# Optimization experiments

Hardware: AMD Instinct MI355X
Metric: run time of the kernel (lower is better)

## Reference

```python
import jax, jax.numpy as jnp
import numpy as np

BATCH = 16384
MODEL_DIM = 768
SAE_HIDDEN = 16384
K = 3


def setup_inputs() -> dict:
    key = jax.random.key(0)
    k1, k2, k3, k4, k5 = jax.random.split(key, 5)
    scale_enc = 1.0 / np.sqrt(MODEL_DIM)
    scale_dec = 1.0 / np.sqrt(SAE_HIDDEN)
    return {
        "model_activations": jax.random.normal(k1, (BATCH, MODEL_DIM), jnp.float32),
        "W_enc": jax.random.normal(k2, (SAE_HIDDEN, MODEL_DIM), jnp.float32) * scale_enc,
        "b_enc": jax.random.normal(k3, (SAE_HIDDEN,), jnp.float32) * scale_enc,
        "W_dec": jax.random.normal(k4, (MODEL_DIM, SAE_HIDDEN), jnp.float32) * scale_dec,
        "b_dec": jax.random.normal(k5, (MODEL_DIM,), jnp.float32) * scale_dec,
    }


def reference(model_activations, W_enc, b_enc, W_dec, b_dec):
    # encoder linear: [B, D] @ [D, H] + [H] -> [B, H]
    pre_activations = model_activations @ W_enc.T + b_enc
    # top-k (k=3) per row
    topk_vals, topk_idx = jax.lax.top_k(pre_activations, K)  # [B, K]
    # scatter the k values into a zero tensor (sparse activation)
    B = pre_activations.shape[0]
    rows = jnp.arange(B)[:, None]  # [B, 1]
    sae_activations = jnp.zeros_like(pre_activations).at[rows, topk_idx].set(topk_vals)
    # number of unique live latents across the whole batch (static-shape version of torch.unique)
    live_mask = jnp.zeros((pre_activations.shape[1],), dtype=jnp.bool_).at[topk_idx.reshape(-1)].set(True)
    num_live_latents = jnp.sum(live_mask.astype(jnp.int32))
    # decoder linear: [B, H] @ [H, D] + [D] -> [B, D]
    reconstructed = sae_activations @ W_dec.T + b_dec
    return reconstructed, num_live_latents
```

## Files before the change

### kernel.cpp

```cpp
#include <hip/hip_runtime.h>
#include <cstdint>
#include <cstddef>

#define B_ROWS 16384
#define DIM    768
#define HID    16384
#define NCB    128
#define KSTEPS (DIM / 32)

typedef __bf16 bf16x8 __attribute__((ext_vector_type(8)));
typedef float  f32x4  __attribute__((ext_vector_type(4)));
typedef unsigned int   u32;
typedef unsigned short u16;

__device__ __forceinline__ u32 umaxu(u32 a, u32 b) { return a > b ? a : b; }
__device__ __forceinline__ u32 uminu(u32 a, u32 b) { return a < b ? a : b; }

__device__ __forceinline__ int swz(int r) { return (r & 3) ^ ((r >> 2) & 3); }

__device__ __forceinline__ u16 f2bf(float f) {
    u32 u = __float_as_uint(f);
    return (u16)((u + 0x7FFFu + ((u >> 16) & 1u)) >> 16);
}

__device__ __forceinline__ u32 pk(float v, int gidx) {
    u32 b = __float_as_uint(v);
    u32 t = b >> 16;
    t ^= (b & 0x80000000u) ? 0xFFFFu : 0x8000u;
    return (t << 16) | (u32)gidx;
}

__device__ __forceinline__ void gll16(const void* g, void* l) {
    __builtin_amdgcn_global_load_lds(
        (const __attribute__((address_space(1))) unsigned int*)g,
        (__attribute__((address_space(3))) unsigned int*)l, 16, 0, 0);
}

__device__ __forceinline__ bool better(float v1, int i1, float v2, int i2) {
    return (v1 > v2) || (v1 == v2 && i1 < i2);
}
__device__ __forceinline__ void ins3(float v, int i,
                                     float& v0, int& i0, float& v1, int& i1,
                                     float& v2, int& i2) {
    if (better(v, i, v2, i2)) {
        v2 = v; i2 = i;
        if (better(v2, i2, v1, i1)) { float tv = v1; int ti = i1; v1 = v2; i1 = i2; v2 = tv; i2 = ti; }
        if (better(v1, i1, v0, i0)) { float tv = v0; int ti = i0; v0 = v1; i0 = i1; v1 = tv; i1 = ti; }
    }
}

__global__ __launch_bounds__(256) void cast_bf16(const float* __restrict__ X,
                                                 const float* __restrict__ W,
                                                 u16* __restrict__ Xb, u16* __restrict__ Wb) {
    const int n4 = (B_ROWS * DIM) / 4;
    for (int i = blockIdx.x * blockDim.x + threadIdx.x; i < n4; i += gridDim.x * blockDim.x) {
        float4 x = ((const float4*)X)[i];
        float4 w = ((const float4*)W)[i];
        ushort4 xo, wo;
        xo.x = f2bf(x.x); xo.y = f2bf(x.y); xo.z = f2bf(x.z); xo.w = f2bf(x.w);
        wo.x = f2bf(w.x); wo.y = f2bf(w.y); wo.z = f2bf(w.z); wo.w = f2bf(w.w);
        ((ushort4*)Xb)[i] = xo;
        ((ushort4*)Wb)[i] = wo;
    }
}

__global__ __launch_bounds__(256) void gemm_screen(const u16* __restrict__ Xb,
                                                   const u16* __restrict__ Wb,
                                                   const float* __restrict__ benc,
                                                   u32* __restrict__ pvpi) {
    __shared__ __align__(16) u16 As[128 * 32];
    __shared__ __align__(16) u16 Bs[128 * 32];
    __shared__ u32 sm[4 * 64 * 3];

    const int bid = blockIdx.x;
    const int st = bid >> 8, loc = bid & 255;
    const int rb = (st >> 3) * 16 + (loc >> 4);
    const int cb = (st & 7) * 16 + (loc & 15);
    const int rowBase = rb * 128, colBase = cb * 128;

    const int tid = threadIdx.x;
    const int w = tid >> 6, lane = tid & 63;

    const u16* gA[2]; const u16* gB[2]; u16* lA[2]; u16* lB[2];
#pragma unroll
    for (int i = 0; i < 2; i++) {
        const int q = w * 2 + i;
        const int p = q * 64 + lane;
        const int r = p >> 2;
        const int c = (p & 3) ^ swz(r);
        gA[i] = Xb + (size_t)(rowBase + r) * DIM + c * 8;
        gB[i] = Wb + (size_t)(colBase + r) * DIM + c * 8;
        lA[i] = As + q * 512;
        lB[i] = Bs + q * 512;
    }

    const int j = lane & 15, g = lane >> 4;
    const int wm = (w >> 1) * 64, wn = (w & 1) * 64;
    int aoff[4], boff[4];
#pragma unroll
    for (int t = 0; t < 4; t++) {
        const int m = wm + t * 16 + j;
        aoff[t] = m * 4 + (g ^ swz(m));
        const int n = wn + t * 16 + j;
        boff[t] = n * 4 + (g ^ swz(n));
    }

    f32x4 acc[4][4];
#pragma unroll
    for (int mt = 0; mt < 4; mt++)
#pragma unroll
        for (int nt = 0; nt < 4; nt++) acc[mt][nt] = (f32x4){0.f, 0.f, 0.f, 0.f};

#pragma unroll
    for (int i = 0; i < 2; i++) { gll16(gA[i], lA[i]); gll16(gB[i], lB[i]); }

    const bf16x8* As8 = (const bf16x8*)As;
    const bf16x8* Bs8 = (const bf16x8*)Bs;

    for (int kk = 0; kk < KSTEPS; ++kk) {
        __syncthreads();
        bf16x8 aF[4], bF[4];
#pragma unroll
        for (int t = 0; t < 4; t++) { aF[t] = As8[aoff[t]]; bF[t] = Bs8[boff[t]]; }
        __syncthreads();
        if (kk + 1 < KSTEPS) {
            const int o = (kk + 1) * 32;
#pragma unroll
            for (int i = 0; i < 2; i++) { gll16(gA[i] + o, lA[i]); gll16(gB[i] + o, lB[i]); }
        }
#pragma unroll
        for (int mt = 0; mt < 4; mt++)
#pragma unroll
            for (int nt = 0; nt < 4; nt++)
                acc[mt][nt] = __builtin_amdgcn_mfma_f32_16x16x32_bf16(aF[mt], bF[nt], acc[mt][nt], 0, 0, 0);
    }

    float bias[4]; int gcol[4];
#pragma unroll
    for (int nt = 0; nt < 4; nt++) {
        gcol[nt] = colBase + wn + nt * 16 + j;
        bias[nt] = benc[gcol[nt]];
    }

#pragma unroll
    for (int mt = 0; mt < 4; mt++) {
#pragma unroll
        for (int reg = 0; reg < 4; reg++) {
            const u32 k0 = pk(acc[mt][0][reg] + bias[0], gcol[0]);
            const u32 k1 = pk(acc[mt][1][reg] + bias[1], gcol[1]);
            const u32 k2 = pk(acc[mt][2][reg] + bias[2], gcol[2]);
            const u32 k3 = pk(acc[mt][3][reg] + bias[3], gcol[3]);
            u32 a0 = umaxu(k0, k1), a1 = uminu(k0, k1);
            u32 b0 = umaxu(k2, k3), b1 = uminu(k2, k3);
            u32 x0 = umaxu(a0, b0);
            u32 p = uminu(a0, b0), q = umaxu(a1, b1), r2 = uminu(a1, b1);
            u32 x1 = umaxu(p, q);
            u32 x2 = umaxu(uminu(p, q), r2);
#pragma unroll
            for (int mk = 1; mk < 16; mk <<= 1) {
                const u32 y0 = (u32)__shfl_xor((int)x0, mk, 64);
                const u32 y1 = (u32)__shfl_xor((int)x1, mk, 64);
                const u32 y2 = (u32)__shfl_xor((int)x2, mk, 64);
                const u32 P = uminu(x0, y0), Q = umaxu(x1, y1);
                const u32 R = uminu(x1, y1), S = umaxu(x2, y2);
                const u32 z0 = umaxu(x0, y0);
                const u32 z1 = umaxu(P, Q);
                const u32 z2 = umaxu(umaxu(uminu(P, Q), R), S);
                x0 = z0; x1 = z1; x2 = z2;
            }
            if ((lane & 15) == 0) {
                const int rloc = mt * 16 + g * 4 + reg;
                sm[(w * 64 + rloc) * 3 + 0] = x0;
                sm[(w * 64 + rloc) * 3 + 1] = x1;
                sm[(w * 64 + rloc) * 3 + 2] = x2;
            }
        }
    }
    __syncthreads();
    if (tid < 128) {
        const int row = tid;
        const int wp = (row >> 6) * 2, rl = row & 63;
        const u32 A0 = sm[((wp + 0) * 64 + rl) * 3 + 0];
        const u32 A1 = sm[((wp + 0) * 64 + rl) * 3 + 1];
        const u32 A2 = sm[((wp + 0) * 64 + rl) * 3 + 2];
        const u32 B0 = sm[((wp + 1) * 64 + rl) * 3 + 0];
        const u32 B1 = sm[((wp + 1) * 64 + rl) * 3 + 1];
        const u32 B2 = sm[((wp + 1) * 64 + rl) * 3 + 2];
        const u32 P = uminu(A0, B0), Q = umaxu(A1, B1);
        const u32 R = uminu(A1, B1), S = umaxu(A2, B2);
        const u32 z0 = umaxu(A0, B0);
        const u32 z1 = umaxu(P, Q);
        const u32 z2 = umaxu(umaxu(uminu(P, Q), R), S);
        const size_t base = ((size_t)(rowBase + row) * NCB + cb) * 3;
        pvpi[base + 0] = z0; pvpi[base + 1] = z1; pvpi[base + 2] = z2;
    }
}

__global__ __launch_bounds__(256) void reduce_recheck(
        const u32* __restrict__ pvpi, const float* __restrict__ X,
        const float* __restrict__ Wenc, const float* __restrict__ benc,
        float* __restrict__ fv, int* __restrict__ fi, int* __restrict__ mask) {
    const int wid = threadIdx.x >> 6, lane = threadIdx.x & 63;
    const int row = blockIdx.x * 4 + wid;

    const u32* p = pvpi + (size_t)row * (NCB * 3);
    u32 k[6];
#pragma unroll
    for (int t = 0; t < 6; t++) k[t] = p[t * 64 + lane];

    u32 cand[16];
#pragma unroll
    for (int it = 0; it < 16; ++it) {
        u32 m = k[0];
#pragma unroll
        for (int t = 1; t < 6; t++) m = umaxu(m, k[t]);
#pragma unroll
        for (int mk = 1; mk < 64; mk <<= 1) m = umaxu(m, (u32)__shfl_xor((int)m, mk, 64));
        cand[it] = m;
#pragma unroll
        for (int t = 0; t < 6; t++) if (k[t] == m) k[t] = 0;
    }

    const float4* xp = (const float4*)(X + (size_t)row * DIM) + lane * 3;
    const float4 x0 = xp[0], x1 = xp[1], x2 = xp[2];

    float v0 = -INFINITY, v1 = -INFINITY, v2 = -INFINITY;
    int   i0 = 0x7fffffff, i1 = 0x7fffffff, i2 = 0x7fffffff;
#pragma unroll
    for (int it = 0; it < 16; ++it) {
        const int ci = (int)(cand[it] & 0xFFFFu);
        const float4* wq = (const float4*)(Wenc + (size_t)ci * DIM) + lane * 3;
        const float4 w0 = wq[0], w1 = wq[1], w2 = wq[2];
        float s = x0.x * w0.x;
        s = fmaf(x0.y, w0.y, s); s = fmaf(x0.z, w0.z, s); s = fmaf(x0.w, w0.w, s);
        s = fmaf(x1.x, w1.x, s); s = fmaf(x1.y, w1.y, s); s = fmaf(x1.z, w1.z, s);
        s = fmaf(x1.w, w1.w, s); s = fmaf(x2.x, w2.x, s); s = fmaf(x2.y, w2.y, s);
        s = fmaf(x2.z, w2.z, s); s = fmaf(x2.w, w2.w, s);
#pragma unroll
        for (int mk = 1; mk < 64; mk <<= 1) s += __shfl_xor(s, mk, 64);
        const float val = s + benc[ci];
        ins3(val, ci, v0, i0, v1, i1, v2, i2);
    }
    if (lane == 0) {
        fv[row * 3 + 0] = v0; fv[row * 3 + 1] = v1; fv[row * 3 + 2] = v2;
        fi[row * 3 + 0] = i0; fi[row * 3 + 1] = i1; fi[row * 3 + 2] = i2;
        mask[i0] = 1; mask[i1] = 1; mask[i2] = 1;
    }
}

__global__ __launch_bounds__(256) void count_live(const int* __restrict__ mask,
                                                  float* __restrict__ outScalar) {
    __shared__ int sd[256];
    const int tid = threadIdx.x;
    int s = 0;
    for (int i = tid; i < HID; i += 256) s += mask[i];
    sd[tid] = s;
    __syncthreads();
    for (int st = 128; st > 0; st >>= 1) {
        if (tid < st) sd[tid] += sd[tid + st];
        __syncthreads();
    }
    if (tid == 0) outScalar[0] = (float)sd[0];
}

__global__ __launch_bounds__(256) void transpose_wdec(const float* __restrict__ W,
                                                      float* __restrict__ Wt) {
    __shared__ float t[32][33];
    const int bx = blockIdx.x;
    const int by = blockIdx.y;
    const int x = threadIdx.x & 31;
    const int y = threadIdx.x >> 5;
#pragma unroll
    for (int i = 0; i < 4; i++) {
        const int d = by * 32 + y + i * 8;
        t[y + i * 8][x] = W[(size_t)d * HID + bx * 32 + x];
    }
    __syncthreads();
#pragma unroll
    for (int i = 0; i < 4; i++) {
        const int h = bx * 32 + y + i * 8;
        Wt[(size_t)h * DIM + by * 32 + x] = t[x][y + i * 8];
    }
}

__global__ __launch_bounds__(192) void decode_rows(
        const float* __restrict__ fv, const int* __restrict__ fi,
        const float* __restrict__ Wt, const float* __restrict__ bdec,
        float* __restrict__ out) {
    const int row = blockIdx.x;
    const int tid = threadIdx.x;
    const float v0 = fv[row * 3 + 0], v1 = fv[row * 3 + 1], v2 = fv[row * 3 + 2];
    const int   i0 = fi[row * 3 + 0], i1 = fi[row * 3 + 1], i2 = fi[row * 3 + 2];
    const int jj = tid * 4;
    const float4 b  = *(const float4*)(bdec + jj);
    const float4 w0 = *(const float4*)(Wt + (size_t)i0 * DIM + jj);
    const float4 w1 = *(const float4*)(Wt + (size_t)i1 * DIM + jj);
    const float4 w2 = *(const float4*)(Wt + (size_t)i2 * DIM + jj);
    float4 o;
    o.x = b.x + v0 * w0.x + v1 * w1.x + v2 * w2.x;
    o.y = b.y + v0 * w0.y + v1 * w1.y + v2 * w2.y;
    o.z = b.z + v0 * w0.z + v1 * w1.z + v2 * w2.z;
    o.w = b.w + v0 * w0.w + v1 * w1.w + v2 * w2.w;
    *(float4*)(out + (size_t)row * DIM + jj) = o;
}

extern "C" void kernel_launch(void* const* d_in, const int* in_sizes, int n_in,
                              void* d_out, int out_size, void* d_ws, size_t ws_size,
                              hipStream_t stream) {
    const float* X    = (const float*)d_in[0];
    const float* Wenc = (const float*)d_in[1];
    const float* benc = (const float*)d_in[2];
    const float* Wdec = (const float*)d_in[3];
    const float* bdec = (const float*)d_in[4];
    float* out = (float*)d_out;

    char* ws = (char*)d_ws;
    u16*   Xb   = (u16*)ws;
    u16*   Wb   = (u16*)(ws + 25165824);
    float* Wt   = (float*)ws;
    u32*   pvpi = (u32*)(ws + 50331648);
    float* fv   = (float*)(ws + 75497472);
    int*   fi   = (int*)(ws + 75694080);
    int*   mask = (int*)(ws + 75890688);

    hipMemsetAsync(mask, 0, HID * sizeof(int), stream);

    cast_bf16<<<3072, 256, 0, stream>>>(X, Wenc, Xb, Wb);
    gemm_screen<<<16384, 256, 0, stream>>>(Xb, Wb, benc, pvpi);
    reduce_recheck<<<B_ROWS / 4, 256, 0, stream>>>(pvpi, X, Wenc, benc, fv, fi, mask);
    count_live<<<1, 256, 0, stream>>>(mask, out + (size_t)B_ROWS * DIM);
    transpose_wdec<<<dim3(HID / 32, DIM / 32), 256, 0, stream>>>(Wdec, Wt);
    decode_rows<<<B_ROWS, 192, 0, stream>>>(fv, fi, Wt, bdec, out);
}
```

Before: 925.8 us.

## Enlarge encoder GEMM tiles to 256x256 with double-buffered pipelined LDS staging

The screening GEMM moves from 128x128x32 tiles with 256 threads to 256x256x64 tiles with 512 threads. LDS is double-buffered with a split-phase schedule that interleaves global-to-LDS loads, LDS reads and MFMA quarters, and MFMA sections run at raised wave priority. Blocks are remapped across 8 groups for cache locality. Halving the column-block count shrinks the candidate buffer and the per-row reduction work in reduce_recheck. The cost is much higher register and LDS pressure and intricate vmcnt/barrier ordering that could limit occupancy or be fragile.

```diff
diff --git a/kernel.cpp b/kernel.cpp
--- a/kernel.cpp
+++ b/kernel.cpp
@@ -5,8 +5,10 @@
 #define B_ROWS 16384
 #define DIM    768
 #define HID    16384
-#define NCB    128
-#define KSTEPS (DIM / 32)
+#define BM     256
+#define BK     64
+#define KT_N   (DIM / BK)
+#define NCB    (HID / BM)
 
 typedef __bf16 bf16x8 __attribute__((ext_vector_type(8)));
 typedef float  f32x4  __attribute__((ext_vector_type(4)));
@@ -15,8 +17,6 @@
 
 __device__ __forceinline__ u32 umaxu(u32 a, u32 b) { return a > b ? a : b; }
 __device__ __forceinline__ u32 uminu(u32 a, u32 b) { return a < b ? a : b; }
-
-__device__ __forceinline__ int swz(int r) { return (r & 3) ^ ((r >> 2) & 3); }
 
 __device__ __forceinline__ u16 f2bf(float f) {
     u32 u = __float_as_uint(f);
@@ -34,6 +34,16 @@
     __builtin_amdgcn_global_load_lds(
         (const __attribute__((address_space(1))) unsigned int*)g,
         (__attribute__((address_space(3))) unsigned int*)l, 16, 0, 0);
+}
+
+__device__ __forceinline__ void merge3(u32& z0, u32& z1, u32& z2,
+                                       u32 A0, u32 A1, u32 A2,
+                                       u32 B0, u32 B1, u32 B2) {
+    const u32 P = uminu(A0, B0), Q = umaxu(A1, B1);
+    const u32 R = uminu(A1, B1), S = umaxu(A2, B2);
+    z0 = umaxu(A0, B0);
+    z1 = umaxu(P, Q);
+    z2 = umaxu(umaxu(uminu(P, Q), R), S);
 }
 
 __device__ __forceinline__ bool better(float v1, int i1, float v2, int i2) {
@@ -64,88 +74,129 @@
     }
 }
 
-__global__ __launch_bounds__(256) void gemm_screen(const u16* __restrict__ Xb,
-                                                   const u16* __restrict__ Wb,
-                                                   const float* __restrict__ benc,
-                                                   u32* __restrict__ pvpi) {
-    __shared__ __align__(16) u16 As[128 * 32];
-    __shared__ __align__(16) u16 Bs[128 * 32];
-    __shared__ u32 sm[4 * 64 * 3];
+__global__ __launch_bounds__(512, 2) void gemm_screen(const u16* __restrict__ Xb,
+                                                      const u16* __restrict__ Wb,
+                                                      const float* __restrict__ benc,
+                                                      u32* __restrict__ pvpi) {
+    __shared__ __align__(16) u16 As[2 * BM * BK];
+    __shared__ __align__(16) u16 Bs[2 * BM * BK];
 
     const int bid = blockIdx.x;
-    const int st = bid >> 8, loc = bid & 255;
-    const int rb = (st >> 3) * 16 + (loc >> 4);
-    const int cb = (st & 7) * 16 + (loc & 15);
-    const int rowBase = rb * 128, colBase = cb * 128;
+    const int wg = ((bid & 7) << 9) | (bid >> 3);
+    const int st = wg >> 8, loc = wg & 255;
+    const int rb = ((st >> 2) << 4) | (loc >> 4);
+    const int cb = ((st & 3) << 4) | (loc & 15);
+    const int rowBase = rb * BM, colBase = cb * BM;
 
     const int tid = threadIdx.x;
-    const int w = tid >> 6, lane = tid & 63;
-
-    const u16* gA[2]; const u16* gB[2]; u16* lA[2]; u16* lB[2];
-#pragma unroll
-    for (int i = 0; i < 2; i++) {
-        const int q = w * 2 + i;
-        const int p = q * 64 + lane;
-        const int r = p >> 2;
-        const int c = (p & 3) ^ swz(r);
-        gA[i] = Xb + (size_t)(rowBase + r) * DIM + c * 8;
-        gB[i] = Wb + (size_t)(colBase + r) * DIM + c * 8;
-        lA[i] = As + q * 512;
-        lB[i] = Bs + q * 512;
-    }
-
+    const int wid = tid >> 6, lane = tid & 63;
+    const int wm = wid >> 2, wn = wid & 3;
     const int j = lane & 15, g = lane >> 4;
-    const int wm = (w >> 1) * 64, wn = (w & 1) * 64;
-    int aoff[4], boff[4];
-#pragma unroll
-    for (int t = 0; t < 4; t++) {
-        const int m = wm + t * 16 + j;
-        aoff[t] = m * 4 + (g ^ swz(m));
-        const int n = wn + t * 16 + j;
-        boff[t] = n * 4 + (g ^ swz(n));
-    }
-
-    f32x4 acc[4][4];
-#pragma unroll
-    for (int mt = 0; mt < 4; mt++)
-#pragma unroll
-        for (int nt = 0; nt < 4; nt++) acc[mt][nt] = (f32x4){0.f, 0.f, 0.f, 0.f};
-
-#pragma unroll
-    for (int i = 0; i < 2; i++) { gll16(gA[i], lA[i]); gll16(gB[i], lB[i]); }
+    const int js = j & 7;
+
+    const int sr = tid >> 3, ss = tid & 7;
+    const int sc = ss ^ (sr & 7);
+    const u32 aoff = (u32)(rowBase + sr) * DIM + (u32)sc * 8;
+    const u32 boff = (u32)(colBase + sr) * DIM + (u32)sc * 8;
+    const int lbw = wid * 512;
+
+#define STAGE_A(H, KTL, D1) do { \
+    gll16(Xb + aoff + (H) * 98304u + (u32)(KTL) * 64u,           As + (D1) * 16384 + (H) * 8192 + lbw); \
+    gll16(Xb + aoff + (H) * 98304u + 49152u + (u32)(KTL) * 64u,  As + (D1) * 16384 + (H) * 8192 + 4096 + lbw); \
+} while (0)
+#define STAGE_B(H, KTL, D1) do { \
+    gll16(Wb + boff + (H) * 98304u + (u32)(KTL) * 64u,           Bs + (D1) * 16384 + (H) * 8192 + lbw); \
+    gll16(Wb + boff + (H) * 98304u + 49152u + (u32)(KTL) * 64u,  Bs + (D1) * 16384 + (H) * 8192 + 4096 + lbw); \
+} while (0)
 
     const bf16x8* As8 = (const bf16x8*)As;
     const bf16x8* Bs8 = (const bf16x8*)Bs;
 
-    for (int kk = 0; kk < KSTEPS; ++kk) {
-        __syncthreads();
-        bf16x8 aF[4], bF[4];
-#pragma unroll
-        for (int t = 0; t < 4; t++) { aF[t] = As8[aoff[t]]; bF[t] = Bs8[boff[t]]; }
-        __syncthreads();
-        if (kk + 1 < KSTEPS) {
-            const int o = (kk + 1) * 32;
-#pragma unroll
-            for (int i = 0; i < 2; i++) { gll16(gA[i] + o, lA[i]); gll16(gB[i] + o, lB[i]); }
-        }
-#pragma unroll
-        for (int mt = 0; mt < 4; mt++)
-#pragma unroll
-            for (int nt = 0; nt < 4; nt++)
-                acc[mt][nt] = __builtin_amdgcn_mfma_f32_16x16x32_bf16(aF[mt], bF[nt], acc[mt][nt], 0, 0, 0);
-    }
+#define READ_A(MH, D) do { \
+    _Pragma("unroll") for (int mtl = 0; mtl < 4; ++mtl) { \
+        const int m8_ = (D) * 2048 + (wm * 128 + ((MH) * 4 + mtl) * 16 + j) * 8; \
+        aF[mtl][0] = As8[m8_ + ((0 + g) ^ js)]; \
+        aF[mtl][1] = As8[m8_ + ((4 + g) ^ js)]; \
+    } } while (0)
+#define READ_B(DST, NH, D) do { \
+    _Pragma("unroll") for (int ntl = 0; ntl < 2; ++ntl) { \
+        const int n8_ = (D) * 2048 + (wn * 64 + ((NH) * 2 + ntl) * 16 + j) * 8; \
+        DST[ntl][0] = Bs8[n8_ + ((0 + g) ^ js)]; \
+        DST[ntl][1] = Bs8[n8_ + ((4 + g) ^ js)]; \
+    } } while (0)
+
+#define MFMA_Q(MH, NH, BF) do { \
+    __builtin_amdgcn_s_setprio(1); \
+    _Pragma("unroll") for (int kk2 = 0; kk2 < 2; ++kk2) \
+    _Pragma("unroll") for (int mtl = 0; mtl < 4; ++mtl) \
+    _Pragma("unroll") for (int ntl = 0; ntl < 2; ++ntl) \
+        acc[(MH) * 4 + mtl][(NH) * 2 + ntl] = __builtin_amdgcn_mfma_f32_16x16x32_bf16( \
+            aF[mtl][kk2], BF[ntl][kk2], acc[(MH) * 4 + mtl][(NH) * 2 + ntl], 0, 0, 0); \
+    __builtin_amdgcn_s_setprio(0); \
+} while (0)
+
+    f32x4 acc[8][4];
+#pragma unroll
+    for (int mt = 0; mt < 8; ++mt)
+#pragma unroll
+        for (int nt = 0; nt < 4; ++nt) acc[mt][nt] = (f32x4){0.f, 0.f, 0.f, 0.f};
+
+    STAGE_A(0, 0, 0); STAGE_B(0, 0, 0); STAGE_B(1, 0, 0); STAGE_A(1, 0, 0);
+    asm volatile("s_waitcnt vmcnt(4)" ::: "memory");
+    __builtin_amdgcn_s_barrier();
+
+    bf16x8 aF[4][2], bLo[2][2], bHi[2][2];
+
+#pragma unroll 1
+    for (int t = 0; t < KT_N; ++t) {
+        const int d = t & 1, d1 = d ^ 1;
+        const bool stg = (t + 1 < KT_N);
+        const int kt = t + 1;
+
+        READ_A(0, d);
+        READ_B(bLo, 0, d);
+        if (stg) STAGE_A(0, kt, d1);
+        __builtin_amdgcn_s_barrier();
+        MFMA_Q(0, 0, bLo);
+        if (stg) asm volatile("s_waitcnt vmcnt(4)" ::: "memory");
+        else     asm volatile("s_waitcnt vmcnt(2)" ::: "memory");
+        __builtin_amdgcn_s_barrier();
+
+        READ_B(bHi, 1, d);
+        if (stg) STAGE_B(0, kt, d1);
+        __builtin_amdgcn_s_barrier();
+        MFMA_Q(0, 1, bHi);
+        if (stg) asm volatile("s_waitcnt vmcnt(4)" ::: "memory");
+        else     asm volatile("s_waitcnt vmcnt(0)" ::: "memory");
+        __builtin_amdgcn_s_barrier();
+
+        READ_A(1, d);
+        if (stg) STAGE_B(1, kt, d1);
+        __builtin_amdgcn_s_barrier();
+        MFMA_Q(1, 1, bHi);
+        __builtin_amdgcn_s_barrier();
+
+        if (stg) STAGE_A(1, kt, d1);
+        __builtin_amdgcn_s_barrier();
+        MFMA_Q(1, 0, bLo);
+        if (stg) asm volatile("s_waitcnt vmcnt(4)" ::: "memory");
+        __builtin_amdgcn_s_barrier();
+    }
+
+    __syncthreads();
+    u32* sm = (u32*)As;
 
     float bias[4]; int gcol[4];
 #pragma unroll
-    for (int nt = 0; nt < 4; nt++) {
-        gcol[nt] = colBase + wn + nt * 16 + j;
+    for (int nt = 0; nt < 4; ++nt) {
+        gcol[nt] = colBase + wn * 64 + nt * 16 + j;
         bias[nt] = benc[gcol[nt]];
     }
 
 #pragma unroll
-    for (int mt = 0; mt < 4; mt++) {
-#pragma unroll
-        for (int reg = 0; reg < 4; reg++) {
+    for (int mt = 0; mt < 8; ++mt) {
+#pragma unroll
+        for (int reg = 0; reg < 4; ++reg) {
             const u32 k0 = pk(acc[mt][0][reg] + bias[0], gcol[0]);
             const u32 k1 = pk(acc[mt][1][reg] + bias[1], gcol[1]);
             const u32 k2 = pk(acc[mt][2][reg] + bias[2], gcol[2]);
@@ -161,39 +212,34 @@
                 const u32 y0 = (u32)__shfl_xor((int)x0, mk, 64);
                 const u32 y1 = (u32)__shfl_xor((int)x1, mk, 64);
                 const u32 y2 = (u32)__shfl_xor((int)x2, mk, 64);
-                const u32 P = uminu(x0, y0), Q = umaxu(x1, y1);
-                const u32 R = uminu(x1, y1), S = umaxu(x2, y2);
-                const u32 z0 = umaxu(x0, y0);
-                const u32 z1 = umaxu(P, Q);
-                const u32 z2 = umaxu(umaxu(uminu(P, Q), R), S);
+                u32 z0, z1, z2;
+                merge3(z0, z1, z2, x0, x1, x2, y0, y1, y2);
                 x0 = z0; x1 = z1; x2 = z2;
             }
             if ((lane & 15) == 0) {
-                const int rloc = mt * 16 + g * 4 + reg;
-                sm[(w * 64 + rloc) * 3 + 0] = x0;
-                sm[(w * 64 + rloc) * 3 + 1] = x1;
-                sm[(w * 64 + rloc) * 3 + 2] = x2;
+                const int row = wm * 128 + mt * 16 + g * 4 + reg;
+                sm[row * 12 + wn * 3 + 0] = x0;
+                sm[row * 12 + wn * 3 + 1] = x1;
+                sm[row * 12 + wn * 3 + 2] = x2;
             }
         }
     }
     __syncthreads();
-    if (tid < 128) {
+    if (tid < 256) {
         const int row = tid;
-        const int wp = (row >> 6) * 2, rl = row & 63;
-        const u32 A0 = sm[((wp + 0) * 64 + rl) * 3 + 0];
-        const u32 A1 = sm[((wp + 0) * 64 + rl) * 3 + 1];
-        const u32 A2 = sm[((wp + 0) * 64 + rl) * 3 + 2];
-        const u32 B0 = sm[((wp + 1) * 64 + rl) * 3 + 0];
-        const u32 B1 = sm[((wp + 1) * 64 + rl) * 3 + 1];
-        const u32 B2 = sm[((wp + 1) * 64 + rl) * 3 + 2];
-        const u32 P = uminu(A0, B0), Q = umaxu(A1, B1);
-        const u32 R = uminu(A1, B1), S = umaxu(A2, B2);
-        const u32 z0 = umaxu(A0, B0);
-        const u32 z1 = umaxu(P, Q);
-        const u32 z2 = umaxu(umaxu(uminu(P, Q), R), S);
+        const u32* s = sm + row * 12;
+        u32 m0, m1, m2, n0, n1, n2, z0, z1, z2;
+        merge3(m0, m1, m2, s[0], s[1], s[2], s[3], s[4], s[5]);
+        merge3(n0, n1, n2, s[6], s[7], s[8], s[9], s[10], s[11]);
+        merge3(z0, z1, z2, m0, m1, m2, n0, n1, n2);
         const size_t base = ((size_t)(rowBase + row) * NCB + cb) * 3;
         pvpi[base + 0] = z0; pvpi[base + 1] = z1; pvpi[base + 2] = z2;
     }
+#undef STAGE_A
+#undef STAGE_B
+#undef READ_A
+#undef READ_B
+#undef MFMA_Q
 }
 
 __global__ __launch_bounds__(256) void reduce_recheck(
@@ -204,21 +250,19 @@
     const int row = blockIdx.x * 4 + wid;
 
     const u32* p = pvpi + (size_t)row * (NCB * 3);
-    u32 k[6];
-#pragma unroll
-    for (int t = 0; t < 6; t++) k[t] = p[t * 64 + lane];
+    u32 k[3];
+#pragma unroll
+    for (int t = 0; t < 3; t++) k[t] = p[t * 64 + lane];
 
     u32 cand[16];
 #pragma unroll
     for (int it = 0; it < 16; ++it) {
-        u32 m = k[0];
-#pragma unroll
-        for (int t = 1; t < 6; t++) m = umaxu(m, k[t]);
+        u32 m = umaxu(umaxu(k[0], k[1]), k[2]);
 #pragma unroll
         for (int mk = 1; mk < 64; mk <<= 1) m = umaxu(m, (u32)__shfl_xor((int)m, mk, 64));
         cand[it] = m;
 #pragma unroll
-        for (int t = 0; t < 6; t++) if (k[t] == m) k[t] = 0;
+        for (int t = 0; t < 3; t++) if (k[t] == m) k[t] = 0;
     }
 
     const float4* xp = (const float4*)(X + (size_t)row * DIM) + lane * 3;
@@ -319,14 +363,14 @@
     u16*   Wb   = (u16*)(ws + 25165824);
     float* Wt   = (float*)ws;
     u32*   pvpi = (u32*)(ws + 50331648);
-    float* fv   = (float*)(ws + 75497472);
-    int*   fi   = (int*)(ws + 75694080);
-    int*   mask = (int*)(ws + 75890688);
+    float* fv   = (float*)(ws + 62914560);
+    int*   fi   = (int*)(ws + 63111168);
+    int*   mask = (int*)(ws + 63307776);
 
     hipMemsetAsync(mask, 0, HID * sizeof(int), stream);
 
     cast_bf16<<<3072, 256, 0, stream>>>(X, Wenc, Xb, Wb);
-    gemm_screen<<<16384, 256, 0, stream>>>(Xb, Wb, benc, pvpi);
+    gemm_screen<<<4096, 512, 0, stream>>>(Xb, Wb, benc, pvpi);
     reduce_recheck<<<B_ROWS / 4, 256, 0, stream>>>(pvpi, X, Wenc, benc, fv, fi, mask);
     count_live<<<1, 256, 0, stream>>>(mask, out + (size_t)B_ROWS * DIM);
     transpose_wdec<<<dim3(HID / 32, DIM / 32), 256, 0, stream>>>(Wdec, Wt);
```

Measured after the change: 858.3 us. -7.3%, faster.
